# Kernel optimization log

Hardware: AMD Instinct MI355X
Metric: run time of the kernel (lower is better)

Reference implementation:

```python
import jax, jax.numpy as jnp
import numpy as np

THETA = 10000.0
NUM_HEADS = 16


def _rope_tables(seq_len, d_k, dtype):
    exponent = jnp.arange(d_k // 2, dtype=jnp.float32) * (2.0 / d_k)
    inv_freq = THETA ** (-exponent)                      # (d_k/2,)
    pos = jnp.arange(seq_len, dtype=jnp.float32)
    angles = pos[:, None] * inv_freq[None, :]            # (n, d_k/2)
    return jnp.cos(angles).astype(dtype), jnp.sin(angles).astype(dtype)


def _apply_rope(x, cos, sin):
    # x: (..., n, d_k); interleaved pair convention: pairs are (x[...,2i], x[...,2i+1])
    x1 = x[..., 0::2]
    x2 = x[..., 1::2]
    r1 = x1 * cos - x2 * sin
    r2 = x1 * sin + x2 * cos
    return jnp.stack([r1, r2], axis=-1).reshape(x.shape)


def setup_inputs() -> dict:
    key = jax.random.key(0)
    ks = jax.random.split(key, 5)
    B, N, D = 2, 4096, 1024
    std = (2.0 / (D + D)) ** 0.5
    return {
        "x": jax.random.normal(ks[0], (B, N, D), dtype=jnp.float32),
        "Wq": jax.random.normal(ks[1], (D, D), dtype=jnp.float32) * std,
        "Wk": jax.random.normal(ks[2], (D, D), dtype=jnp.float32) * std,
        "Wv": jax.random.normal(ks[3], (D, D), dtype=jnp.float32) * std,
        "Wo": jax.random.normal(ks[4], (D, D), dtype=jnp.float32) * std,
    }


def reference(x, Wq, Wk, Wv, Wo):
    B, N, D = x.shape
    H = NUM_HEADS
    d_k = D // H

    def proj(W):
        y = jnp.einsum('oi,bni->bno', W, x)
        return y.reshape(B, N, H, d_k).transpose(0, 2, 1, 3)  # (b,h,n,d)

    Q, K, V = proj(Wq), proj(Wk), proj(Wv)

    cos, sin = _rope_tables(N, d_k, x.dtype)
    Q = _apply_rope(Q, cos, sin)
    K = _apply_rope(K, cos, sin)

    scores = jnp.einsum('bhnd,bhmd->bhnm', Q, K) / jnp.sqrt(jnp.asarray(d_k, x.dtype))
    causal = jnp.tril(jnp.ones((N, N), dtype=bool))
    scores = jnp.where(causal, scores, -jnp.inf)
    attn = jax.nn.softmax(scores, axis=-1)
    out = jnp.einsum('bhnm,bhmd->bhnd', attn, V)          # (b,h,n,d)
    out = out.transpose(0, 2, 1, 3).reshape(B, N, D)
    return jnp.einsum('oi,bni->bno', Wo, out)
```

## Files before the change

kernel.cpp:

```cpp
#include <hip/hip_runtime.h>
#include <hip/hip_bf16.h>
#include <stdint.h>

typedef __attribute__((ext_vector_type(8))) short short8;
typedef __attribute__((ext_vector_type(4))) float f32x4;

#define NSEQ 4096
#define DMODEL 1024
#define MROWS 8192

__device__ __forceinline__ unsigned short f2bf(float f) {
  union { float f; unsigned u; } v; v.f = f;
  unsigned r = v.u + 0x7fffu + ((v.u >> 16) & 1u);
  return (unsigned short)(r >> 16);
}

__device__ __forceinline__ unsigned pk2(float lo, float hi) {
  unsigned short a = __bfloat16_as_ushort(__float2bfloat16(lo));
  unsigned short b = __bfloat16_as_ushort(__float2bfloat16(hi));
  return ((unsigned)b << 16) | (unsigned)a;
}

__device__ __forceinline__ void gload16(const unsigned short* g, unsigned short* l) {
  __builtin_amdgcn_global_load_lds(
      (const __attribute__((address_space(1))) unsigned int*)g,
      (__attribute__((address_space(3))) unsigned int*)l, 16, 0, 0);
}

__global__ void k_conv(const float* __restrict__ src, unsigned short* __restrict__ dst) {
  int i = (blockIdx.x * 256 + threadIdx.x) * 4;
  float4 v = *(const float4*)(src + i);
  ushort4 o;
  o.x = f2bf(v.x); o.y = f2bf(v.y); o.z = f2bf(v.z); o.w = f2bf(v.w);
  *(ushort4*)(dst + i) = o;
}

__global__ void k_convw(const float* __restrict__ s0, const float* __restrict__ s1,
                        const float* __restrict__ s2, const float* __restrict__ s3,
                        unsigned short* __restrict__ dst) {
  int z = blockIdx.x >> 10;
  const float* src = (z == 0) ? s0 : (z == 1) ? s1 : (z == 2) ? s2 : s3;
  float sc = (z == 0) ? 0.18033688011112042f : 1.0f;
  int i = ((blockIdx.x & 1023) * 256 + threadIdx.x) * 4;
  float4 v = *(const float4*)(src + i);
  ushort4 o;
  o.x = f2bf(v.x * sc); o.y = f2bf(v.y * sc); o.z = f2bf(v.z * sc); o.w = f2bf(v.w * sc);
  *(ushort4*)(dst + (size_t)z * 1048576 + i) = o;
}

__global__ void k_rope_tab(float* __restrict__ cosT, float* __restrict__ sinT) {
  int i = blockIdx.x * 256 + threadIdx.x;
  int pos = i >> 5, j = i & 31;
  float invf = exp2f(-(float)j * 0.41524101186092029f);
  float ang = (float)pos * invf;
  cosT[i] = cosf(ang);
  sinT[i] = sinf(ang);
}

__global__ __launch_bounds__(256) void k_gemm_bt(
    const unsigned short* __restrict__ A,
    const unsigned short* __restrict__ Bw,
    unsigned short* __restrict__ obf,
    unsigned short* __restrict__ Vt,
    float* __restrict__ of32,
    const float* __restrict__ cosT, const float* __restrict__ sinT,
    int K, int modeArg) {
  const int N = DMODEL;
  const int q8 = gridDim.x >> 3;
  const int wg = (blockIdx.x & 7) * q8 + (blockIdx.x >> 3);
  const int z = wg >> 9;
  const int rr = wg & 511;
  const int bn = rr & 7, bm = rr >> 3;
  const int mode = (modeArg < 0) ? z : modeArg;
  const unsigned short* Bz = Bw + (size_t)z * DMODEL * K;
  unsigned short* oz = (obf && mode <= 1) ? (obf + (size_t)z * MROWS * DMODEL) : nullptr;

  const int t = threadIdx.x;
  const int w = t >> 6, lane = t & 63;
  const int wr = w >> 1, wc = w & 1;
  const int lr = lane & 15, lg = lane >> 4;

  __shared__ __align__(16) unsigned short SM[2][128 * 64];
  unsigned short* Al = SM[0];
  unsigned short* Bl = SM[1];

  const unsigned short* Ab = A + (size_t)bm * 128 * K;
  const unsigned short* Bb = Bz + (size_t)bn * 128 * K;
  const int trow = t >> 3, tcol = (t & 7) * 8;

  f32x4 acc[4][4] = {};

  for (int k0 = 0; k0 < K; k0 += 64) {
#pragma unroll
    for (int c = 0; c < 4; ++c) {
      gload16(Ab + (size_t)(c * 32 + trow) * K + k0 + tcol, &Al[c * 2048 + t * 8]);
      gload16(Bb + (size_t)(c * 32 + trow) * K + k0 + tcol, &Bl[c * 2048 + t * 8]);
    }
    asm volatile("s_waitcnt vmcnt(0)" ::: "memory");
    __syncthreads();
#pragma unroll
    for (int kk = 0; kk < 2; ++kk) {
      short8 af[4], bfr[4];
#pragma unroll
      for (int mi = 0; mi < 4; ++mi)
        af[mi] = *(const short8*)&Al[(wr * 64 + mi * 16 + lr) * 64 + kk * 32 + lg * 8];
#pragma unroll
      for (int ni = 0; ni < 4; ++ni)
        bfr[ni] = *(const short8*)&Bl[(wc * 64 + ni * 16 + lr) * 64 + kk * 32 + lg * 8];
#pragma unroll
      for (int mi = 0; mi < 4; ++mi)
#pragma unroll
        for (int ni = 0; ni < 4; ++ni)
          acc[mi][ni] = __builtin_amdgcn_mfma_f32_16x16x32_bf16(af[mi], bfr[ni], acc[mi][ni], 0, 0, 0);
    }
    __syncthreads();
  }

  if (mode <= 1 || mode == 3) {
    float* Cf = (float*)&SM[0][0];
#pragma unroll
    for (int half = 0; half < 2; ++half) {
      if (half) __syncthreads();
      if (wr == half) {
#pragma unroll
        for (int mi = 0; mi < 4; ++mi)
#pragma unroll
          for (int ni = 0; ni < 4; ++ni)
#pragma unroll
            for (int r = 0; r < 4; ++r) {
              int row = mi * 16 + lg * 4 + r;
              int col = (wc * 64 + ni * 16 + lr) ^ (lg << 3);
              Cf[row * 128 + col] = acc[mi][ni][r];
            }
      }
      __syncthreads();
      int pr = t >> 2;
      int gm = bm * 128 + half * 64 + pr;
      int xorv = ((pr >> 2) & 3) << 3;
      if (mode == 3) {
        float* orow = of32 + (size_t)gm * N + bn * 128;
#pragma unroll
        for (int k = 0; k < 4; ++k) {
          int c0 = (t & 3) * 8 + k * 32;
          int cs = c0 ^ xorv;
          float4 va = *(const float4*)&Cf[pr * 128 + cs];
          float4 vb = *(const float4*)&Cf[pr * 128 + cs + 4];
          *(float4*)(orow + c0) = va;
          *(float4*)(orow + c0 + 4) = vb;
        }
      } else {
        int pos = gm & (NSEQ - 1);
        const float* cB = cosT + pos * 32;
        const float* sB = sinT + pos * 32;
        unsigned short* orow = oz + (size_t)gm * N + bn * 128;
#pragma unroll
        for (int k = 0; k < 4; ++k) {
          int c0 = (t & 3) * 8 + k * 32;
          int cs = c0 ^ xorv;
          float4 va = *(const float4*)&Cf[pr * 128 + cs];
          float4 vb = *(const float4*)&Cf[pr * 128 + cs + 4];
          int j0 = (c0 & 63) >> 1;
          float4 cv = *(const float4*)&cB[j0];
          float4 sv = *(const float4*)&sB[j0];
          uint4 o;
          o.x = pk2(va.x * cv.x - va.y * sv.x, va.x * sv.x + va.y * cv.x);
          o.y = pk2(va.z * cv.y - va.w * sv.y, va.z * sv.y + va.w * cv.y);
          o.z = pk2(vb.x * cv.z - vb.y * sv.z, vb.x * sv.z + vb.y * cv.z);
          o.w = pk2(vb.z * cv.w - vb.w * sv.w, vb.z * sv.w + vb.w * cv.w);
          *(uint4*)(orow + c0) = o;
        }
      }
    }
  } else {
#pragma unroll
    for (int mi = 0; mi < 4; ++mi)
#pragma unroll
      for (int ni = 0; ni < 4; ++ni) {
        int gm0 = bm * 128 + wr * 64 + mi * 16 + lg * 4;
        int gn = bn * 128 + wc * 64 + ni * 16 + lr;
        int b = gm0 >> 12, n = gm0 & (NSEQ - 1);
        int h = gn >> 6, d = gn & 63;
        uint2 u;
        u.x = pk2(acc[mi][ni][0], acc[mi][ni][1]);
        u.y = pk2(acc[mi][ni][2], acc[mi][ni][3]);
        *(uint2*)(Vt + ((size_t)((b * 16 + h) * 64 + d)) * NSEQ + n) = u;
      }
  }
}

__global__ __launch_bounds__(256, 2) void k_attn6(
    const unsigned short* __restrict__ Qb,
    const unsigned short* __restrict__ Kb,
    const unsigned short* __restrict__ Vtg,
    unsigned short* __restrict__ AO) {
  const int id = blockIdx.x;
  const int bh = id & 31;
  const int pq = id >> 5;
  const int b = bh >> 4, h = bh & 15;
  const int t = threadIdx.x;
  const int w = t >> 6, lane = t & 63;
  const int lr = lane & 15, hi4 = lane >> 4;
  const size_t rowbase = (size_t)b * NSEQ;

  __shared__ __align__(16) unsigned short Kl[2][64 * 64];
  __shared__ __align__(16) unsigned short Vl[2][64 * 64];
  __shared__ __align__(16) unsigned short Pl[4][16 * 64];

  const int pswz = (lr & 7) << 3;

  short8 ones;
#pragma unroll
  for (int i = 0; i < 8; ++i) ones[i] = (short)0x3F80;

#define STAGE(buf, kv0)                                                                   \
  {                                                                                       \
    _Pragma("unroll")                                                                     \
    for (int it = 0; it < 2; ++it) {                                                      \
      int c = t + it * 256;                                                               \
      int row = c >> 3, sg = (c & 7) ^ (row & 7);                                         \
      gload16(Kb + (rowbase + (kv0) + row) * DMODEL + h * 64 + sg * 8, &Kl[buf][c * 8]);  \
      gload16(Vtg + ((size_t)bh * 64 + row) * NSEQ + (kv0) + sg * 8, &Vl[buf][c * 8]);    \
    }                                                                                     \
  }

#pragma unroll
  for (int qi = 0; qi < 2; ++qi) {
    const int qt = qi ? pq : (31 - pq);
    const int q0w = qt * 128 + w * 32;

    short8 qf[2][2];
#pragma unroll
    for (int sub = 0; sub < 2; ++sub) {
      const unsigned short* qp = Qb + (rowbase + q0w + sub * 16 + lr) * DMODEL + h * 64 + hi4 * 8;
#pragma unroll
      for (int s = 0; s < 2; ++s)
        qf[sub][s] = *(const short8*)(qp + s * 32);
    }

    f32x4 oacc[2][4] = {};
    f32x4 lacc[2] = {};
    const int nkv = (qt + 1) * 2;

    STAGE(0, 0);
    asm volatile("s_waitcnt vmcnt(0)" ::: "memory");
    __syncthreads();

    for (int ib = 0; ib < nkv; ++ib) {
      const int kv0 = ib * 64, cur = ib & 1;
      if (ib + 1 < nkv) STAGE(cur ^ 1, kv0 + 64);

      if (kv0 <= q0w + 31) {
        short8 Kf[4][2], Vf[2][4];
#pragma unroll
        for (int t4 = 0; t4 < 4; ++t4)
#pragma unroll
          for (int s = 0; s < 2; ++s)
            Kf[t4][s] = *(const short8*)&Kl[cur][(t4 * 16 + lr) * 64 + (((s * 4 + hi4) ^ (lr & 7)) * 8)];
#pragma unroll
        for (int c = 0; c < 2; ++c)
#pragma unroll
          for (int dt = 0; dt < 4; ++dt)
            Vf[c][dt] = *(const short8*)&Vl[cur][(dt * 16 + lr) * 64 + (((c * 4 + hi4) ^ (lr & 7)) * 8)];

#pragma unroll
        for (int sub = 0; sub < 2; ++sub) {
          const int qs = q0w + sub * 16;
          const int qlane = qs + lr;
          f32x4 sa[4];
          const f32x4 zz = {0.f, 0.f, 0.f, 0.f};
          __builtin_amdgcn_s_setprio(1);
#pragma unroll
          for (int t4 = 0; t4 < 4; ++t4) {
            f32x4 x = __builtin_amdgcn_mfma_f32_16x16x32_bf16(Kf[t4][0], qf[sub][0], zz, 0, 0, 0);
            sa[t4] = __builtin_amdgcn_mfma_f32_16x16x32_bf16(Kf[t4][1], qf[sub][1], x, 0, 0, 0);
          }
          __builtin_amdgcn_s_setprio(0);
          if (kv0 + 63 > qs) {
#pragma unroll
            for (int t4 = 0; t4 < 4; ++t4)
#pragma unroll
              for (int r = 0; r < 4; ++r)
                if (kv0 + t4 * 16 + hi4 * 4 + r > qlane) sa[t4][r] = -1e30f;
          }
#pragma unroll
          for (int t4 = 0; t4 < 4; ++t4)
#pragma unroll
            for (int r = 0; r < 4; ++r)
              sa[t4][r] = __builtin_amdgcn_exp2f(sa[t4][r]);
#pragma unroll
          for (int t4 = 0; t4 < 4; ++t4) {
            uint2 u;
            u.x = pk2(sa[t4][0], sa[t4][1]);
            u.y = pk2(sa[t4][2], sa[t4][3]);
            *(uint2*)&Pl[w][lr * 64 + ((t4 * 16 + hi4 * 4) ^ pswz)] = u;
          }
          asm volatile("s_waitcnt lgkmcnt(0)" ::: "memory");
          __builtin_amdgcn_sched_barrier(0);
          short8 pf0 = *(const short8*)&Pl[w][lr * 64 + ((hi4 * 8) ^ pswz)];
          short8 pf1 = *(const short8*)&Pl[w][lr * 64 + ((32 + hi4 * 8) ^ pswz)];
          __builtin_amdgcn_s_setprio(1);
#pragma unroll
          for (int dt = 0; dt < 4; ++dt) {
            oacc[sub][dt] = __builtin_amdgcn_mfma_f32_16x16x32_bf16(Vf[0][dt], pf0, oacc[sub][dt], 0, 0, 0);
            oacc[sub][dt] = __builtin_amdgcn_mfma_f32_16x16x32_bf16(Vf[1][dt], pf1, oacc[sub][dt], 0, 0, 0);
          }
          lacc[sub] = __builtin_amdgcn_mfma_f32_16x16x32_bf16(ones, pf0, lacc[sub], 0, 0, 0);
          lacc[sub] = __builtin_amdgcn_mfma_f32_16x16x32_bf16(ones, pf1, lacc[sub], 0, 0, 0);
          __builtin_amdgcn_s_setprio(0);
        }
      }
      asm volatile("s_waitcnt vmcnt(0)" ::: "memory");
      __syncthreads();
    }

#pragma unroll
    for (int sub = 0; sub < 2; ++sub) {
      float inv = 1.f / lacc[sub][0];
#pragma unroll
      for (int dt = 0; dt < 4; ++dt) {
        uint2 u;
        u.x = pk2(oacc[sub][dt][0] * inv, oacc[sub][dt][1] * inv);
        u.y = pk2(oacc[sub][dt][2] * inv, oacc[sub][dt][3] * inv);
        *(uint2*)&Pl[w][lr * 64 + ((dt * 16 + hi4 * 4) ^ pswz)] = u;
      }
      asm volatile("s_waitcnt lgkmcnt(0)" ::: "memory");
      __builtin_amdgcn_sched_barrier(0);
      int q2 = lane >> 2, ch = (lane & 3) * 16;
      int qswz = (q2 & 7) << 3;
      uint4 r0 = *(const uint4*)&Pl[w][q2 * 64 + (ch ^ qswz)];
      uint4 r1 = *(const uint4*)&Pl[w][q2 * 64 + ((ch + 8) ^ qswz)];
      unsigned short* op = AO + (rowbase + q0w + sub * 16 + q2) * DMODEL + h * 64 + ch;
      *(uint4*)op = r0;
      *(uint4*)(op + 8) = r1;
    }
  }
}

extern "C" void kernel_launch(void* const* d_in, const int* in_sizes, int n_in,
                              void* d_out, int out_size, void* d_ws, size_t ws_size,
                              hipStream_t stream) {
  const float* x  = (const float*)d_in[0];
  const float* Wq = (const float*)d_in[1];
  const float* Wk = (const float*)d_in[2];
  const float* Wv = (const float*)d_in[3];
  const float* Wo = (const float*)d_in[4];
  float* out = (float*)d_out;
  char* ws = (char*)d_ws;

  unsigned short* xb  = (unsigned short*)(ws);
  unsigned short* Wb  = (unsigned short*)(ws + 16777216);
  unsigned short* Qb  = (unsigned short*)(ws + 25165824);
  unsigned short* Kb  = Qb + 8388608;
  unsigned short* Vtg = (unsigned short*)(ws + 58720256);
  unsigned short* AO  = (unsigned short*)(ws + 75497472);
  float* cosT = (float*)(ws + 92274688);
  float* sinT = (float*)(ws + 92798976);

  k_conv<<<8192, 256, 0, stream>>>(x, xb);
  k_convw<<<4096, 256, 0, stream>>>(Wq, Wk, Wv, Wo, Wb);
  k_rope_tab<<<512, 256, 0, stream>>>(cosT, sinT);

  k_gemm_bt<<<1536, 256, 0, stream>>>(xb, Wb, Qb, Vtg, nullptr, cosT, sinT, DMODEL, -1);

  k_attn6<<<512, 256, 0, stream>>>(Qb, Kb, Vtg, AO);

  k_gemm_bt<<<512, 256, 0, stream>>>(AO, Wb + 3145728, nullptr, nullptr, out, cosT, sinT, DMODEL, 3);
}
```

Measured before the change: 230.9 us.

## Stage 128-wide KV tiles per barrier and batch P writes across sub-tiles

```diff
diff --git a/kernel.cpp b/kernel.cpp
--- a/kernel.cpp
+++ b/kernel.cpp
@@ -188,7 +188,7 @@
   }
 }
 
-__global__ __launch_bounds__(256, 2) void k_attn6(
+__global__ __launch_bounds__(256, 2) void k_attn7(
     const unsigned short* __restrict__ Qb,
     const unsigned short* __restrict__ Kb,
     const unsigned short* __restrict__ Vtg,
@@ -202,9 +202,9 @@
   const int lr = lane & 15, hi4 = lane >> 4;
   const size_t rowbase = (size_t)b * NSEQ;
 
-  __shared__ __align__(16) unsigned short Kl[2][64 * 64];
-  __shared__ __align__(16) unsigned short Vl[2][64 * 64];
-  __shared__ __align__(16) unsigned short Pl[4][16 * 64];
+  __shared__ __align__(16) unsigned short Kl[2][128 * 64];
+  __shared__ __align__(16) unsigned short Vl[2][64 * 128];
+  __shared__ __align__(16) unsigned short Pl[4][2][16 * 64];
 
   const int pswz = (lr & 7) << 3;
 
@@ -212,15 +212,17 @@
 #pragma unroll
   for (int i = 0; i < 8; ++i) ones[i] = (short)0x3F80;
 
-#define STAGE(buf, kv0)                                                                   \
-  {                                                                                       \
-    _Pragma("unroll")                                                                     \
-    for (int it = 0; it < 2; ++it) {                                                      \
-      int c = t + it * 256;                                                               \
-      int row = c >> 3, sg = (c & 7) ^ (row & 7);                                         \
-      gload16(Kb + (rowbase + (kv0) + row) * DMODEL + h * 64 + sg * 8, &Kl[buf][c * 8]);  \
-      gload16(Vtg + ((size_t)bh * 64 + row) * NSEQ + (kv0) + sg * 8, &Vl[buf][c * 8]);    \
-    }                                                                                     \
+#define STAGE(buf, kv0)                                                                        \
+  {                                                                                            \
+    _Pragma("unroll")                                                                          \
+    for (int c = 0; c < 4; ++c) {                                                              \
+      int rK = c * 32 + (t >> 3);                                                              \
+      int sgK = ((t & 7) ^ (rK & 7)) * 8;                                                      \
+      gload16(Kb + (rowbase + (kv0) + rK) * DMODEL + h * 64 + sgK, &Kl[buf][c * 2048 + t * 8]);\
+      int rV = c * 16 + (t >> 4);                                                              \
+      int sgV = ((t & 15) ^ (rV & 7)) * 8;                                                     \
+      gload16(Vtg + ((size_t)bh * 64 + rV) * NSEQ + (kv0) + sgV, &Vl[buf][c * 2048 + t * 8]);  \
+    }                                                                                          \
   }
 
 #pragma unroll
@@ -239,76 +241,92 @@
 
     f32x4 oacc[2][4] = {};
     f32x4 lacc[2] = {};
-    const int nkv = (qt + 1) * 2;
+    const int nkv = qt + 1;
 
     STAGE(0, 0);
     asm volatile("s_waitcnt vmcnt(0)" ::: "memory");
     __syncthreads();
 
     for (int ib = 0; ib < nkv; ++ib) {
-      const int kv0 = ib * 64, cur = ib & 1;
-      if (ib + 1 < nkv) STAGE(cur ^ 1, kv0 + 64);
-
-      if (kv0 <= q0w + 31) {
-        short8 Kf[4][2], Vf[2][4];
-#pragma unroll
-        for (int t4 = 0; t4 < 4; ++t4)
-#pragma unroll
-          for (int s = 0; s < 2; ++s)
-            Kf[t4][s] = *(const short8*)&Kl[cur][(t4 * 16 + lr) * 64 + (((s * 4 + hi4) ^ (lr & 7)) * 8)];
-#pragma unroll
-        for (int c = 0; c < 2; ++c)
-#pragma unroll
-          for (int dt = 0; dt < 4; ++dt)
-            Vf[c][dt] = *(const short8*)&Vl[cur][(dt * 16 + lr) * 64 + (((c * 4 + hi4) ^ (lr & 7)) * 8)];
-
-#pragma unroll
-        for (int sub = 0; sub < 2; ++sub) {
-          const int qs = q0w + sub * 16;
-          const int qlane = qs + lr;
-          f32x4 sa[4];
-          const f32x4 zz = {0.f, 0.f, 0.f, 0.f};
+      const int cur = ib & 1;
+      if (ib + 1 < nkv) STAGE(cur ^ 1, (ib + 1) * 128);
+
+#pragma unroll
+      for (int hh = 0; hh < 2; ++hh) {
+        const int kv0h = ib * 128 + hh * 64;
+        if (kv0h <= q0w + 31) {
+          short8 Kf[4][2];
+#pragma unroll
+          for (int t4 = 0; t4 < 4; ++t4)
+#pragma unroll
+            for (int s = 0; s < 2; ++s)
+              Kf[t4][s] = *(const short8*)&Kl[cur][(hh * 64 + t4 * 16 + lr) * 64 + (((s * 4 + hi4) ^ (lr & 7)) * 8)];
+
+#pragma unroll
+          for (int sub = 0; sub < 2; ++sub) {
+            const int qs = q0w + sub * 16;
+            const int qlane = qs + lr;
+            f32x4 sa[4];
+            const f32x4 zz = {0.f, 0.f, 0.f, 0.f};
+            __builtin_amdgcn_s_setprio(1);
+#pragma unroll
+            for (int t4 = 0; t4 < 4; ++t4) {
+              f32x4 x = __builtin_amdgcn_mfma_f32_16x16x32_bf16(Kf[t4][0], qf[sub][0], zz, 0, 0, 0);
+              sa[t4] = __builtin_amdgcn_mfma_f32_16x16x32_bf16(Kf[t4][1], qf[sub][1], x, 0, 0, 0);
+            }
+            __builtin_amdgcn_s_setprio(0);
+            if (kv0h + 63 > qs) {
+#pragma unroll
+              for (int t4 = 0; t4 < 4; ++t4)
+#pragma unroll
+                for (int r = 0; r < 4; ++r)
+                  if (kv0h + t4 * 16 + hi4 * 4 + r > qlane) sa[t4][r] = -1e30f;
+            }
+#pragma unroll
+            for (int t4 = 0; t4 < 4; ++t4)
+#pragma unroll
+              for (int r = 0; r < 4; ++r)
+                sa[t4][r] = __builtin_amdgcn_exp2f(sa[t4][r]);
+#pragma unroll
+            for (int t4 = 0; t4 < 4; ++t4) {
+              uint2 u;
+              u.x = pk2(sa[t4][0], sa[t4][1]);
+              u.y = pk2(sa[t4][2], sa[t4][3]);
+              *(uint2*)&Pl[w][sub][lr * 64 + ((t4 * 16 + hi4 * 4) ^ pswz)] = u;
+            }
+          }
+
+          short8 Vf[2][4];
+#pragma unroll
+          for (int c = 0; c < 2; ++c)
+#pragma unroll
+            for (int dt = 0; dt < 4; ++dt)
+              Vf[c][dt] = *(const short8*)&Vl[cur][(dt * 16 + lr) * 128 + (((hh * 8 + c * 4 + hi4) ^ (lr & 7)) * 8)];
+
+          asm volatile("s_waitcnt lgkmcnt(0)" ::: "memory");
+          __builtin_amdgcn_sched_barrier(0);
+
+          short8 pf[2][2];
+#pragma unroll
+          for (int sub = 0; sub < 2; ++sub) {
+            pf[sub][0] = *(const short8*)&Pl[w][sub][lr * 64 + ((hi4 * 8) ^ pswz)];
+            pf[sub][1] = *(const short8*)&Pl[w][sub][lr * 64 + ((32 + hi4 * 8) ^ pswz)];
+          }
           __builtin_amdgcn_s_setprio(1);
 #pragma unroll
-          for (int t4 = 0; t4 < 4; ++t4) {
-            f32x4 x = __builtin_amdgcn_mfma_f32_16x16x32_bf16(Kf[t4][0], qf[sub][0], zz, 0, 0, 0);
-            sa[t4] = __builtin_amdgcn_mfma_f32_16x16x32_bf16(Kf[t4][1], qf[sub][1], x, 0, 0, 0);
+          for (int sub = 0; sub < 2; ++sub) {
+#pragma unroll
+            for (int dt = 0; dt < 4; ++dt) {
+              oacc[sub][dt] = __builtin_amdgcn_mfma_f32_16x16x32_bf16(Vf[0][dt], pf[sub][0], oacc[sub][dt], 0, 0, 0);
+              oacc[sub][dt] = __builtin_amdgcn_mfma_f32_16x16x32_bf16(Vf[1][dt], pf[sub][1], oacc[sub][dt], 0, 0, 0);
+            }
+            lacc[sub] = __builtin_amdgcn_mfma_f32_16x16x32_bf16(ones, pf[sub][0], lacc[sub], 0, 0, 0);
+            lacc[sub] = __builtin_amdgcn_mfma_f32_16x16x32_bf16(ones, pf[sub][1], lacc[sub], 0, 0, 0);
           }
           __builtin_amdgcn_s_setprio(0);
-          if (kv0 + 63 > qs) {
-#pragma unroll
-            for (int t4 = 0; t4 < 4; ++t4)
-#pragma unroll
-              for (int r = 0; r < 4; ++r)
-                if (kv0 + t4 * 16 + hi4 * 4 + r > qlane) sa[t4][r] = -1e30f;
-          }
-#pragma unroll
-          for (int t4 = 0; t4 < 4; ++t4)
-#pragma unroll
-            for (int r = 0; r < 4; ++r)
-              sa[t4][r] = __builtin_amdgcn_exp2f(sa[t4][r]);
-#pragma unroll
-          for (int t4 = 0; t4 < 4; ++t4) {
-            uint2 u;
-            u.x = pk2(sa[t4][0], sa[t4][1]);
-            u.y = pk2(sa[t4][2], sa[t4][3]);
-            *(uint2*)&Pl[w][lr * 64 + ((t4 * 16 + hi4 * 4) ^ pswz)] = u;
-          }
-          asm volatile("s_waitcnt lgkmcnt(0)" ::: "memory");
-          __builtin_amdgcn_sched_barrier(0);
-          short8 pf0 = *(const short8*)&Pl[w][lr * 64 + ((hi4 * 8) ^ pswz)];
-          short8 pf1 = *(const short8*)&Pl[w][lr * 64 + ((32 + hi4 * 8) ^ pswz)];
-          __builtin_amdgcn_s_setprio(1);
-#pragma unroll
-          for (int dt = 0; dt < 4; ++dt) {
-            oacc[sub][dt] = __builtin_amdgcn_mfma_f32_16x16x32_bf16(Vf[0][dt], pf0, oacc[sub][dt], 0, 0, 0);
-            oacc[sub][dt] = __builtin_amdgcn_mfma_f32_16x16x32_bf16(Vf[1][dt], pf1, oacc[sub][dt], 0, 0, 0);
-          }
-          lacc[sub] = __builtin_amdgcn_mfma_f32_16x16x32_bf16(ones, pf0, lacc[sub], 0, 0, 0);
-          lacc[sub] = __builtin_amdgcn_mfma_f32_16x16x32_bf16(ones, pf1, lacc[sub], 0, 0, 0);
-          __builtin_amdgcn_s_setprio(0);
         }
       }
+
       asm volatile("s_waitcnt vmcnt(0)" ::: "memory");
       __syncthreads();
     }
@@ -321,14 +339,17 @@
         uint2 u;
         u.x = pk2(oacc[sub][dt][0] * inv, oacc[sub][dt][1] * inv);
         u.y = pk2(oacc[sub][dt][2] * inv, oacc[sub][dt][3] * inv);
-        *(uint2*)&Pl[w][lr * 64 + ((dt * 16 + hi4 * 4) ^ pswz)] = u;
-      }
-      asm volatile("s_waitcnt lgkmcnt(0)" ::: "memory");
-      __builtin_amdgcn_sched_barrier(0);
+        *(uint2*)&Pl[w][sub][lr * 64 + ((dt * 16 + hi4 * 4) ^ pswz)] = u;
+      }
+    }
+    asm volatile("s_waitcnt lgkmcnt(0)" ::: "memory");
+    __builtin_amdgcn_sched_barrier(0);
+#pragma unroll
+    for (int sub = 0; sub < 2; ++sub) {
       int q2 = lane >> 2, ch = (lane & 3) * 16;
       int qswz = (q2 & 7) << 3;
-      uint4 r0 = *(const uint4*)&Pl[w][q2 * 64 + (ch ^ qswz)];
-      uint4 r1 = *(const uint4*)&Pl[w][q2 * 64 + ((ch + 8) ^ qswz)];
+      uint4 r0 = *(const uint4*)&Pl[w][sub][q2 * 64 + (ch ^ qswz)];
+      uint4 r1 = *(const uint4*)&Pl[w][sub][q2 * 64 + ((ch + 8) ^ qswz)];
       unsigned short* op = AO + (rowbase + q0w + sub * 16 + q2) * DMODEL + h * 64 + ch;
       *(uint4*)op = r0;
       *(uint4*)(op + 8) = r1;
@@ -362,7 +383,7 @@
 
   k_gemm_bt<<<1536, 256, 0, stream>>>(xb, Wb, Qb, Vtg, nullptr, cosT, sinT, DMODEL, -1);
 
-  k_attn6<<<512, 256, 0, stream>>>(Qb, Kb, Vtg, AO);
+  k_attn7<<<512, 256, 0, stream>>>(Qb, Kb, Vtg, AO);
 
   k_gemm_bt<<<512, 256, 0, stream>>>(AO, Wb + 3145728, nullptr, nullptr, out, cosT, sinT, DMODEL, 3);
 }
```

Measured after the change: 234.3 us. No clear change (+1.5%).
